# Optimization experiments

Measured on AMD Instinct MI355X. Metric: run time of the kernel, lower is better.

Reference implementation:

```python
import jax, jax.numpy as jnp
import numpy as np
from jax import lax

EPS = 1e-8
TAU = 1.0  # step=0 < tau_warmup_steps -> tau = tau_init


def setup_inputs() -> dict:
    key = jax.random.key(0)
    k1, k2 = jax.random.split(key)
    B, D, H, W = 4, 256, 32, 32
    C, K, d = 8, 1024, 32  # n_codebooks, vocab_size, codebook_dim (D = C*d)
    z = jax.random.normal(k1, (B, D, H, W), dtype=jnp.float32)
    cb = jax.random.normal(k2, (C, K, d), dtype=jnp.float32)
    cb = cb / (jnp.linalg.norm(cb, axis=-1, keepdims=True) + 1e-12) * np.sqrt(d).astype(np.float32)
    return {"z": z, "codebooks": cb}


def reference(z, codebooks):
    # Training-mode forward of LGQuantizer (step=0).
    B, D, H, W = z.shape
    C, K, d = codebooks.shape
    # (b d h w) -> (b h w) (c d_sub): chunk along channel dim
    zf = z.transpose(0, 2, 3, 1).reshape(-1, C, d)  # [N, C, d]
    N = zf.shape[0]

    # pairwise squared distances per codebook: [N, C, K]
    z_sq = jnp.sum(zf * zf, axis=-1)                      # [N, C]
    cb_sq = jnp.sum(codebooks * codebooks, axis=-1)       # [C, K]
    cross = jnp.einsum('ncd,ckd->nck', zf, codebooks)     # [N, C, K]
    dists = z_sq[:, :, None] - 2.0 * cross + cb_sq[None, :, :]

    inv_temp = 1.0 / (2.0 * TAU * TAU + EPS)
    logits = -dists * inv_temp
    q = jax.nn.softmax(logits, axis=-1)                   # [N, C, K]

    # soft quantization + straight-through with hard lookup
    z_q = jnp.einsum('nck,ckd->ncd', q, codebooks)        # [N, C, d]
    idx = jnp.argmin(dists, axis=-1)                      # [N, C]
    z_q_hard = codebooks[jnp.arange(C)[None, :], idx]     # [N, C, d]
    z_q_st = z_q + lax.stop_gradient(z_q_hard - z_q)

    quantized = z_q_st.reshape(B, H, W, D).transpose(0, 3, 1, 2)  # [B, D, H, W]
    indices = idx.reshape(B, H, W, C).transpose(0, 3, 1, 2)       # [B, C, H, W]

    # commitment: mse(z_part, q.detach() @ cb.detach()), averaged over codebooks
    commitment = jnp.mean((zf - lax.stop_gradient(z_q)) ** 2)

    log_q = jnp.log(q + EPS)
    neg_ent = jnp.sum(q * log_q, axis=-1)                 # [N, C]
    expected_dist = jnp.mean(jnp.sum(q * dists, axis=-1), axis=0)  # [C]
    kl_uniform = jnp.mean(neg_ent, axis=0) + np.log(K).astype(np.float32)  # [C]
    free_energy = jnp.mean(expected_dist * inv_temp + kl_uniform)

    confidence_loss = jnp.mean(-neg_ent)

    q_bar = jnp.mean(q, axis=0)                           # [C, K]
    balance_loss = jnp.mean(jnp.sum(q_bar * jnp.log(q_bar * K + EPS), axis=-1))

    return (quantized, indices, q, commitment, free_energy,
            confidence_loss, balance_loss, jnp.float32(TAU))
```

## Files before the change

kernel.cpp:

```cpp
#include <hip/hip_runtime.h>

#define WS_A0 0
#define WS_A1 1
#define WS_A2 2
#define WS_QBAR 16
#define WS_CBSQ (WS_QBAR + 8192)
#define WS_IDX  (WS_CBSQ + 8192)

#define OUT_IDX  1048576
#define OUT_Q    1081344
#define OUT_SCAL 34635776

__global__ __launch_bounds__(256) void k_cbsq(const float* __restrict__ cb,
                                              float* __restrict__ ws_f) {
  int i = blockIdx.x * 256 + threadIdx.x;
  const float* r = cb + (size_t)i * 32;
  float s = 0.f;
#pragma unroll
  for (int d = 0; d < 32; ++d) s = fmaf(r[d], r[d], s);
  ws_f[WS_CBSQ + i] = s;
}

__device__ __forceinline__ float wsum64(float v) {
#pragma unroll
  for (int m = 32; m >= 1; m >>= 1) v += __shfl_xor(v, m, 64);
  return v;
}

__device__ __forceinline__ float uread(float v) {
  return __int_as_float(__builtin_amdgcn_readfirstlane(__float_as_int(v)));
}

#define ZLD 33
__global__ __launch_bounds__(1024, 4)
void k_main(
    const float* __restrict__ z, const float* __restrict__ cb,
    float* __restrict__ out, float* __restrict__ ws_f, int* __restrict__ ws_i) {
  __shared__ __attribute__((aligned(16))) float smem[39040];
  float* cb_lds   = smem;
  float* qsum     = smem + 32768;
  float* cbsq_lds = smem + 33792;
  float* z_lds    = smem + 34816;

  const int c    = blockIdx.x >> 5;
  const int nblk = blockIdx.x & 31;
  const int tid  = threadIdx.x;
  const int lane = tid & 63;
  const int wave = tid >> 6;

  const int bb   = (nblk * 128) >> 10;
  const int hwb  = (nblk * 128) & 1023;

  const float4* cb4 = (const float4*)(cb + (size_t)c * 32768);
  float4* lds4 = (float4*)cb_lds;
#pragma unroll
  for (int i = 0; i < 8; ++i) {
    int idx = i * 1024 + tid;
    int k = idx >> 3, q = idx & 7;
    lds4[(k << 3) + (q ^ (k & 7))] = cb4[idx];
  }
  qsum[tid] = 0.f;
  cbsq_lds[tid] = ws_f[WS_CBSQ + c * 1024 + tid];
  {
    const float* zbase = z + (((size_t)bb * 256 + c * 32) << 10) + hwb;
#pragma unroll
    for (int i = 0; i < 4; ++i) {
      int idx = i * 1024 + tid;
      int d = idx >> 7, j = idx & 127;
      z_lds[j * ZLD + d] = zbase[(size_t)d * 1024 + j];
    }
  }
  __syncthreads();

  float* out_q   = out + OUT_Q;
  float* out_idx = out + OUT_IDX;

  float accA0 = 0.f, accA1 = 0.f, accA2 = 0.f;
  const int kl7 = lane & 7;

#pragma unroll 1
  for (int pp = 0; pp < 4; ++pp) {
    const int nl0 = wave * 8 + pp * 2;
    const int nl1 = nl0 + 1;
    const int n0 = nblk * 128 + nl0;
    const int n1 = n0 + 1;

    float zv0[32], zv1[32];
#pragma unroll
    for (int d = 0; d < 32; ++d) {
      zv0[d] = uread(z_lds[nl0 * ZLD + d]);
      zv1[d] = uread(z_lds[nl1 * ZLD + d]);
    }
    float zs0 = 0.f, zs1 = 0.f;
#pragma unroll
    for (int d = 0; d < 32; ++d) {
      zs0 = fmaf(zv0[d], zv0[d], zs0);
      zs1 = fmaf(zv1[d], zv1[d], zs1);
    }

    float S0 = 0.f, S1 = 0.f, es0 = 0.f, es1 = 0.f;
    float zqA0[16], zqA1[16];
#pragma unroll
    for (int i = 0; i < 16; ++i) { zqA0[i] = 0.f; zqA1[i] = 0.f; }

#pragma unroll 1
    for (int jj = 0; jj < 16; ++jj) {
      const int k = jj * 64 + lane;
      const int kbase = k << 3;
      float a0 = 0.f, a1 = 0.f, g0 = 0.f, g1 = 0.f;
#pragma unroll
      for (int q = 0; q < 8; ++q) {
        float4 r4 = lds4[kbase + (q ^ kl7)];
        a0 = fmaf(r4.x, zv0[q * 4 + 0], a0);
        a1 = fmaf(r4.y, zv0[q * 4 + 1], a1);
        a0 = fmaf(r4.z, zv0[q * 4 + 2], a0);
        a1 = fmaf(r4.w, zv0[q * 4 + 3], a1);
        g0 = fmaf(r4.x, zv1[q * 4 + 0], g0);
        g1 = fmaf(r4.y, zv1[q * 4 + 1], g1);
        g0 = fmaf(r4.z, zv1[q * 4 + 2], g0);
        g1 = fmaf(r4.w, zv1[q * 4 + 3], g1);
      }
      float cq = cbsq_lds[k];
      float s0 = (a0 + a1) - 0.5f * cq;
      float s1 = (g0 + g1) - 0.5f * cq;
      float ev0 = __expf(s0), ev1 = __expf(s1);
      S0 += ev0;  S1 += ev1;
      es0 = fmaf(ev0, s0, es0);
      es1 = fmaf(ev1, s1, es1);
#pragma unroll
      for (int q = 0; q < 4; ++q) {
        float4 r4 = lds4[kbase + (q ^ kl7)];
        zqA0[q * 4 + 0] = fmaf(ev0, r4.x, zqA0[q * 4 + 0]);
        zqA0[q * 4 + 1] = fmaf(ev0, r4.y, zqA0[q * 4 + 1]);
        zqA0[q * 4 + 2] = fmaf(ev0, r4.z, zqA0[q * 4 + 2]);
        zqA0[q * 4 + 3] = fmaf(ev0, r4.w, zqA0[q * 4 + 3]);
        zqA1[q * 4 + 0] = fmaf(ev1, r4.x, zqA1[q * 4 + 0]);
        zqA1[q * 4 + 1] = fmaf(ev1, r4.y, zqA1[q * 4 + 1]);
        zqA1[q * 4 + 2] = fmaf(ev1, r4.z, zqA1[q * 4 + 2]);
        zqA1[q * 4 + 3] = fmaf(ev1, r4.w, zqA1[q * 4 + 3]);
      }
    }

    float St0 = wsum64(S0), St1 = wsum64(S1);
    float rS0 = 1.f / St0, rS1 = 1.f / St1;
    float est0 = wsum64(es0), est1 = wsum64(es1);

    accA1 += (zs0 - 2.f * est0 * rS0) + (zs1 - 2.f * est1 * rS1);
    accA2 += (est0 * rS0 - __logf(St0)) + (est1 * rS1 - __logf(St1));

    {
#pragma unroll
      for (int t = 0; t < 4; ++t) {
        const int half = 8 >> t;
        const int up = (lane >> (5 - t)) & 1;
#pragma unroll
        for (int i = 0; i < half; ++i) {
          float sa0 = up ? zqA0[i] : zqA0[i + half];
          float ka0 = up ? zqA0[i + half] : zqA0[i];
          zqA0[i] = ka0 + __shfl_xor(sa0, 32 >> t, 64);
          float sa1 = up ? zqA1[i] : zqA1[i + half];
          float ka1 = up ? zqA1[i + half] : zqA1[i];
          zqA1[i] = ka1 + __shfl_xor(sa1, 32 >> t, 64);
        }
      }
      zqA0[0] += __shfl_xor(zqA0[0], 2, 64);
      zqA0[0] += __shfl_xor(zqA0[0], 1, 64);
      zqA1[0] += __shfl_xor(zqA1[0], 2, 64);
      zqA1[0] += __shfl_xor(zqA1[0], 1, 64);
      const int ddA = (lane >> 2) & 15;
      float dA0 = z_lds[nl0 * ZLD + ddA] - zqA0[0] * rS0;
      float dA1 = z_lds[nl1 * ZLD + ddA] - zqA1[0] * rS1;
      accA0 += 0.25f * wsum64(dA0 * dA0 + dA1 * dA1);
    }

    float sm0 = -INFINITY, sm1 = -INFINITY;
    int km0 = 0, km1 = 0;
    float zqB0[16], zqB1[16];
#pragma unroll
    for (int i = 0; i < 16; ++i) { zqB0[i] = 0.f; zqB1[i] = 0.f; }
    float* qp0 = out_q + ((size_t)n0 * 8 + c) * 1024;
    float* qp1 = out_q + ((size_t)n1 * 8 + c) * 1024;

#pragma unroll 1
    for (int jj = 0; jj < 16; ++jj) {
      const int k = jj * 64 + lane;
      const int kbase = k << 3;
      float a0 = 0.f, a1 = 0.f, g0 = 0.f, g1 = 0.f;
#pragma unroll
      for (int q = 0; q < 8; ++q) {
        float4 r4 = lds4[kbase + (q ^ kl7)];
        a0 = fmaf(r4.x, zv0[q * 4 + 0], a0);
        a1 = fmaf(r4.y, zv0[q * 4 + 1], a1);
        a0 = fmaf(r4.z, zv0[q * 4 + 2], a0);
        a1 = fmaf(r4.w, zv0[q * 4 + 3], a1);
        g0 = fmaf(r4.x, zv1[q * 4 + 0], g0);
        g1 = fmaf(r4.y, zv1[q * 4 + 1], g1);
        g0 = fmaf(r4.z, zv1[q * 4 + 2], g0);
        g1 = fmaf(r4.w, zv1[q * 4 + 3], g1);
      }
      float cq = cbsq_lds[k];
      float s0 = (a0 + a1) - 0.5f * cq;
      float s1 = (g0 + g1) - 0.5f * cq;
      if (s0 > sm0) { sm0 = s0; km0 = k; }
      if (s1 > sm1) { sm1 = s1; km1 = k; }
      float qv0 = __expf(s0) * rS0;
      float qv1 = __expf(s1) * rS1;
      __builtin_nontemporal_store(qv0, qp0 + jj * 64 + lane);
      __builtin_nontemporal_store(qv1, qp1 + jj * 64 + lane);
      atomicAdd(&qsum[jj * 64 + lane], qv0 + qv1);
#pragma unroll
      for (int q = 4; q < 8; ++q) {
        float4 r4 = lds4[kbase + (q ^ kl7)];
        const int i0 = (q - 4) * 4;
        zqB0[i0 + 0] = fmaf(qv0, r4.x, zqB0[i0 + 0]);
        zqB0[i0 + 1] = fmaf(qv0, r4.y, zqB0[i0 + 1]);
        zqB0[i0 + 2] = fmaf(qv0, r4.z, zqB0[i0 + 2]);
        zqB0[i0 + 3] = fmaf(qv0, r4.w, zqB0[i0 + 3]);
        zqB1[i0 + 0] = fmaf(qv1, r4.x, zqB1[i0 + 0]);
        zqB1[i0 + 1] = fmaf(qv1, r4.y, zqB1[i0 + 1]);
        zqB1[i0 + 2] = fmaf(qv1, r4.z, zqB1[i0 + 2]);
        zqB1[i0 + 3] = fmaf(qv1, r4.w, zqB1[i0 + 3]);
      }
    }

#pragma unroll
    for (int m = 32; m >= 1; m >>= 1) {
      float so = __shfl_xor(sm0, m, 64); int ko = __shfl_xor(km0, m, 64);
      if (so > sm0 || (so == sm0 && ko < km0)) { sm0 = so; km0 = ko; }
      float sp = __shfl_xor(sm1, m, 64); int kp = __shfl_xor(km1, m, 64);
      if (sp > sm1 || (sp == sm1 && kp < km1)) { sm1 = sp; km1 = kp; }
    }
    if (lane == 0) {
      out_idx[(size_t)bb * 8192 + c * 1024 + hwb + nl0] = (float)km0;
      ws_i[WS_IDX + n0 * 8 + c] = km0;
      out_idx[(size_t)bb * 8192 + c * 1024 + hwb + nl1] = (float)km1;
      ws_i[WS_IDX + n1 * 8 + c] = km1;
    }

#pragma unroll
    for (int t = 0; t < 4; ++t) {
      const int half = 8 >> t;
      const int up = (lane >> (5 - t)) & 1;
#pragma unroll
      for (int i = 0; i < half; ++i) {
        float sa0 = up ? zqB0[i] : zqB0[i + half];
        float ka0 = up ? zqB0[i + half] : zqB0[i];
        zqB0[i] = ka0 + __shfl_xor(sa0, 32 >> t, 64);
        float sa1 = up ? zqB1[i] : zqB1[i + half];
        float ka1 = up ? zqB1[i + half] : zqB1[i];
        zqB1[i] = ka1 + __shfl_xor(sa1, 32 >> t, 64);
      }
    }
    zqB0[0] += __shfl_xor(zqB0[0], 2, 64);
    zqB0[0] += __shfl_xor(zqB0[0], 1, 64);
    zqB1[0] += __shfl_xor(zqB1[0], 2, 64);
    zqB1[0] += __shfl_xor(zqB1[0], 1, 64);
    const int ddB = (lane >> 2) & 15;
    float dB0 = z_lds[nl0 * ZLD + 16 + ddB] - zqB0[0];
    float dB1 = z_lds[nl1 * ZLD + 16 + ddB] - zqB1[0];
    accA0 += 0.25f * wsum64(dB0 * dB0 + dB1 * dB1);
  }

  if (lane == 0) {
    atomicAdd(&ws_f[WS_A0], accA0);
    atomicAdd(&ws_f[WS_A1], accA1);
    atomicAdd(&ws_f[WS_A2], accA2);
  }

  __syncthreads();
  atomicAdd(&ws_f[WS_QBAR + c * 1024 + tid], qsum[tid]);
}

__global__ __launch_bounds__(256) void k_hard(const float* __restrict__ cb,
                                              const int* __restrict__ ws_i,
                                              float* __restrict__ out0) {
  int o = blockIdx.x * 256 + threadIdx.x;
  int b  = o >> 18;
  int r  = o & 262143;
  int ch = r >> 10;
  int hw = r & 1023;
  int c = ch >> 5, dd = ch & 31;
  int n = (b << 10) + hw;
  int k = ws_i[WS_IDX + n * 8 + c];
  out0[o] = cb[((size_t)(c << 10) + k) * 32 + dd];
}

__global__ __launch_bounds__(256) void k_final(const float* __restrict__ ws_f,
                                               float* __restrict__ out_s) {
  __shared__ float red[256];
  int tid = threadIdx.x;
  float bal = 0.f;
  for (int i = tid; i < 8192; i += 256) {
    float qb = ws_f[WS_QBAR + i] * (1.0f / 4096.0f);
    bal += qb * __logf(qb * 1024.0f + 1e-8f);
  }
  red[tid] = bal;
  __syncthreads();
  for (int s = 128; s > 0; s >>= 1) {
    if (tid < s) red[tid] += red[tid + s];
    __syncthreads();
  }
  if (tid == 0) {
    float A0 = ws_f[WS_A0], A1 = ws_f[WS_A1], A2 = ws_f[WS_A2];
    out_s[0] = A0 * (1.0f / 1048576.0f);
    out_s[1] = (0.5f * A1 + A2) * (1.0f / 32768.0f) + 6.93147180559945f;
    out_s[2] = -A2 * (1.0f / 32768.0f);
    out_s[3] = red[0] * 0.125f;
    out_s[4] = 1.0f;
  }
}

extern "C" void kernel_launch(void* const* d_in, const int* in_sizes, int n_in,
                              void* d_out, int out_size, void* d_ws, size_t ws_size,
                              hipStream_t stream) {
  (void)in_sizes; (void)n_in; (void)out_size; (void)ws_size;
  const float* z  = (const float*)d_in[0];
  const float* cb = (const float*)d_in[1];
  float* out  = (float*)d_out;
  float* ws_f = (float*)d_ws;
  int*   ws_i = (int*)d_ws;

  hipMemsetAsync(d_ws, 0, (WS_QBAR + 8192) * sizeof(float), stream);
  k_cbsq <<<32,   256, 0, stream>>>(cb, ws_f);
  k_main <<<256, 1024, 0, stream>>>(z, cb, out, ws_f, ws_i);
  k_hard <<<4096, 256, 0, stream>>>(cb, ws_i, out);
  k_final<<<1,    256, 0, stream>>>(ws_f, out + OUT_SCAL);
}
```

Measured before the change: 481.7 us.

## Fuse cbsq into main kernel, fold final reduction into hard lookup, reuse codebook loads

```diff
diff --git a/kernel.cpp b/kernel.cpp
--- a/kernel.cpp
+++ b/kernel.cpp
@@ -10,16 +10,6 @@
 #define OUT_IDX  1048576
 #define OUT_Q    1081344
 #define OUT_SCAL 34635776
-
-__global__ __launch_bounds__(256) void k_cbsq(const float* __restrict__ cb,
-                                              float* __restrict__ ws_f) {
-  int i = blockIdx.x * 256 + threadIdx.x;
-  const float* r = cb + (size_t)i * 32;
-  float s = 0.f;
-#pragma unroll
-  for (int d = 0; d < 32; ++d) s = fmaf(r[d], r[d], s);
-  ws_f[WS_CBSQ + i] = s;
-}
 
 __device__ __forceinline__ float wsum64(float v) {
 #pragma unroll
@@ -60,7 +50,6 @@
     lds4[(k << 3) + (q ^ (k & 7))] = cb4[idx];
   }
   qsum[tid] = 0.f;
-  cbsq_lds[tid] = ws_f[WS_CBSQ + c * 1024 + tid];
   {
     const float* zbase = z + (((size_t)bb * 256 + c * 32) << 10) + hwb;
 #pragma unroll
@@ -69,6 +58,18 @@
       int d = idx >> 7, j = idx & 127;
       z_lds[j * ZLD + d] = zbase[(size_t)d * 1024 + j];
     }
+  }
+  __syncthreads();
+  {
+    float s = 0.f;
+    const int t7 = tid & 7;
+#pragma unroll
+    for (int q = 0; q < 8; ++q) {
+      float4 r4 = lds4[(tid << 3) + (q ^ t7)];
+      s = fmaf(r4.x, r4.x, s); s = fmaf(r4.y, r4.y, s);
+      s = fmaf(r4.z, r4.z, s); s = fmaf(r4.w, r4.w, s);
+    }
+    cbsq_lds[tid] = s;
   }
   __syncthreads();
 
@@ -109,7 +110,8 @@
       const int kbase = k << 3;
       float a0 = 0.f, a1 = 0.f, g0 = 0.f, g1 = 0.f;
 #pragma unroll
-      for (int q = 0; q < 8; ++q) {
+      for (int qq = 0; qq < 6; ++qq) {
+        const int q = (qq + 4) & 7;
         float4 r4 = lds4[kbase + (q ^ kl7)];
         a0 = fmaf(r4.x, zv0[q * 4 + 0], a0);
         a1 = fmaf(r4.y, zv0[q * 4 + 1], a1);
@@ -120,6 +122,17 @@
         g0 = fmaf(r4.z, zv1[q * 4 + 2], g0);
         g1 = fmaf(r4.w, zv1[q * 4 + 3], g1);
       }
+      float4 kq2 = lds4[kbase + (2 ^ kl7)];
+      a0 = fmaf(kq2.x, zv0[8], a0);  a1 = fmaf(kq2.y, zv0[9], a1);
+      a0 = fmaf(kq2.z, zv0[10], a0); a1 = fmaf(kq2.w, zv0[11], a1);
+      g0 = fmaf(kq2.x, zv1[8], g0);  g1 = fmaf(kq2.y, zv1[9], g1);
+      g0 = fmaf(kq2.z, zv1[10], g0); g1 = fmaf(kq2.w, zv1[11], g1);
+      float4 kq3 = lds4[kbase + (3 ^ kl7)];
+      a0 = fmaf(kq3.x, zv0[12], a0); a1 = fmaf(kq3.y, zv0[13], a1);
+      a0 = fmaf(kq3.z, zv0[14], a0); a1 = fmaf(kq3.w, zv0[15], a1);
+      g0 = fmaf(kq3.x, zv1[12], g0); g1 = fmaf(kq3.y, zv1[13], g1);
+      g0 = fmaf(kq3.z, zv1[14], g0); g1 = fmaf(kq3.w, zv1[15], g1);
+
       float cq = cbsq_lds[k];
       float s0 = (a0 + a1) - 0.5f * cq;
       float s1 = (g0 + g1) - 0.5f * cq;
@@ -128,7 +141,7 @@
       es0 = fmaf(ev0, s0, es0);
       es1 = fmaf(ev1, s1, es1);
 #pragma unroll
-      for (int q = 0; q < 4; ++q) {
+      for (int q = 0; q < 2; ++q) {
         float4 r4 = lds4[kbase + (q ^ kl7)];
         zqA0[q * 4 + 0] = fmaf(ev0, r4.x, zqA0[q * 4 + 0]);
         zqA0[q * 4 + 1] = fmaf(ev0, r4.y, zqA0[q * 4 + 1]);
@@ -139,6 +152,14 @@
         zqA1[q * 4 + 2] = fmaf(ev1, r4.z, zqA1[q * 4 + 2]);
         zqA1[q * 4 + 3] = fmaf(ev1, r4.w, zqA1[q * 4 + 3]);
       }
+      zqA0[8]  = fmaf(ev0, kq2.x, zqA0[8]);  zqA0[9]  = fmaf(ev0, kq2.y, zqA0[9]);
+      zqA0[10] = fmaf(ev0, kq2.z, zqA0[10]); zqA0[11] = fmaf(ev0, kq2.w, zqA0[11]);
+      zqA1[8]  = fmaf(ev1, kq2.x, zqA1[8]);  zqA1[9]  = fmaf(ev1, kq2.y, zqA1[9]);
+      zqA1[10] = fmaf(ev1, kq2.z, zqA1[10]); zqA1[11] = fmaf(ev1, kq2.w, zqA1[11]);
+      zqA0[12] = fmaf(ev0, kq3.x, zqA0[12]); zqA0[13] = fmaf(ev0, kq3.y, zqA0[13]);
+      zqA0[14] = fmaf(ev0, kq3.z, zqA0[14]); zqA0[15] = fmaf(ev0, kq3.w, zqA0[15]);
+      zqA1[12] = fmaf(ev1, kq3.x, zqA1[12]); zqA1[13] = fmaf(ev1, kq3.y, zqA1[13]);
+      zqA1[14] = fmaf(ev1, kq3.z, zqA1[14]); zqA1[15] = fmaf(ev1, kq3.w, zqA1[15]);
     }
 
     float St0 = wsum64(S0), St1 = wsum64(S1);
@@ -187,7 +208,7 @@
       const int kbase = k << 3;
       float a0 = 0.f, a1 = 0.f, g0 = 0.f, g1 = 0.f;
 #pragma unroll
-      for (int q = 0; q < 8; ++q) {
+      for (int q = 0; q < 6; ++q) {
         float4 r4 = lds4[kbase + (q ^ kl7)];
         a0 = fmaf(r4.x, zv0[q * 4 + 0], a0);
         a1 = fmaf(r4.y, zv0[q * 4 + 1], a1);
@@ -198,6 +219,17 @@
         g0 = fmaf(r4.z, zv1[q * 4 + 2], g0);
         g1 = fmaf(r4.w, zv1[q * 4 + 3], g1);
       }
+      float4 kq6 = lds4[kbase + (6 ^ kl7)];
+      a0 = fmaf(kq6.x, zv0[24], a0); a1 = fmaf(kq6.y, zv0[25], a1);
+      a0 = fmaf(kq6.z, zv0[26], a0); a1 = fmaf(kq6.w, zv0[27], a1);
+      g0 = fmaf(kq6.x, zv1[24], g0); g1 = fmaf(kq6.y, zv1[25], g1);
+      g0 = fmaf(kq6.z, zv1[26], g0); g1 = fmaf(kq6.w, zv1[27], g1);
+      float4 kq7 = lds4[kbase + (7 ^ kl7)];
+      a0 = fmaf(kq7.x, zv0[28], a0); a1 = fmaf(kq7.y, zv0[29], a1);
+      a0 = fmaf(kq7.z, zv0[30], a0); a1 = fmaf(kq7.w, zv0[31], a1);
+      g0 = fmaf(kq7.x, zv1[28], g0); g1 = fmaf(kq7.y, zv1[29], g1);
+      g0 = fmaf(kq7.z, zv1[30], g0); g1 = fmaf(kq7.w, zv1[31], g1);
+
       float cq = cbsq_lds[k];
       float s0 = (a0 + a1) - 0.5f * cq;
       float s1 = (g0 + g1) - 0.5f * cq;
@@ -209,7 +241,7 @@
       __builtin_nontemporal_store(qv1, qp1 + jj * 64 + lane);
       atomicAdd(&qsum[jj * 64 + lane], qv0 + qv1);
 #pragma unroll
-      for (int q = 4; q < 8; ++q) {
+      for (int q = 4; q < 6; ++q) {
         float4 r4 = lds4[kbase + (q ^ kl7)];
         const int i0 = (q - 4) * 4;
         zqB0[i0 + 0] = fmaf(qv0, r4.x, zqB0[i0 + 0]);
@@ -221,6 +253,14 @@
         zqB1[i0 + 2] = fmaf(qv1, r4.z, zqB1[i0 + 2]);
         zqB1[i0 + 3] = fmaf(qv1, r4.w, zqB1[i0 + 3]);
       }
+      zqB0[8]  = fmaf(qv0, kq6.x, zqB0[8]);  zqB0[9]  = fmaf(qv0, kq6.y, zqB0[9]);
+      zqB0[10] = fmaf(qv0, kq6.z, zqB0[10]); zqB0[11] = fmaf(qv0, kq6.w, zqB0[11]);
+      zqB1[8]  = fmaf(qv1, kq6.x, zqB1[8]);  zqB1[9]  = fmaf(qv1, kq6.y, zqB1[9]);
+      zqB1[10] = fmaf(qv1, kq6.z, zqB1[10]); zqB1[11] = fmaf(qv1, kq6.w, zqB1[11]);
+      zqB0[12] = fmaf(qv0, kq7.x, zqB0[12]); zqB0[13] = fmaf(qv0, kq7.y, zqB0[13]);
+      zqB0[14] = fmaf(qv0, kq7.z, zqB0[14]); zqB0[15] = fmaf(qv0, kq7.w, zqB0[15]);
+      zqB1[12] = fmaf(qv1, kq7.x, zqB1[12]); zqB1[13] = fmaf(qv1, kq7.y, zqB1[13]);
+      zqB1[14] = fmaf(qv1, kq7.z, zqB1[14]); zqB1[15] = fmaf(qv1, kq7.w, zqB1[15]);
     }
 
 #pragma unroll
@@ -273,7 +313,9 @@
 
 __global__ __launch_bounds__(256) void k_hard(const float* __restrict__ cb,
                                               const int* __restrict__ ws_i,
-                                              float* __restrict__ out0) {
+                                              float* __restrict__ out0,
+                                              const float* __restrict__ ws_f,
+                                              float* __restrict__ out_s) {
   int o = blockIdx.x * 256 + threadIdx.x;
   int b  = o >> 18;
   int r  = o & 262143;
@@ -283,30 +325,29 @@
   int n = (b << 10) + hw;
   int k = ws_i[WS_IDX + n * 8 + c];
   out0[o] = cb[((size_t)(c << 10) + k) * 32 + dd];
-}
-
-__global__ __launch_bounds__(256) void k_final(const float* __restrict__ ws_f,
-                                               float* __restrict__ out_s) {
-  __shared__ float red[256];
-  int tid = threadIdx.x;
-  float bal = 0.f;
-  for (int i = tid; i < 8192; i += 256) {
-    float qb = ws_f[WS_QBAR + i] * (1.0f / 4096.0f);
-    bal += qb * __logf(qb * 1024.0f + 1e-8f);
-  }
-  red[tid] = bal;
-  __syncthreads();
-  for (int s = 128; s > 0; s >>= 1) {
-    if (tid < s) red[tid] += red[tid + s];
+
+  if (blockIdx.x == 0) {
+    __shared__ float red[256];
+    int tid = threadIdx.x;
+    float bal = 0.f;
+    for (int i = tid; i < 8192; i += 256) {
+      float qb = ws_f[WS_QBAR + i] * (1.0f / 4096.0f);
+      bal += qb * __logf(qb * 1024.0f + 1e-8f);
+    }
+    red[tid] = bal;
     __syncthreads();
-  }
-  if (tid == 0) {
-    float A0 = ws_f[WS_A0], A1 = ws_f[WS_A1], A2 = ws_f[WS_A2];
-    out_s[0] = A0 * (1.0f / 1048576.0f);
-    out_s[1] = (0.5f * A1 + A2) * (1.0f / 32768.0f) + 6.93147180559945f;
-    out_s[2] = -A2 * (1.0f / 32768.0f);
-    out_s[3] = red[0] * 0.125f;
-    out_s[4] = 1.0f;
+    for (int s = 128; s > 0; s >>= 1) {
+      if (tid < s) red[tid] += red[tid + s];
+      __syncthreads();
+    }
+    if (tid == 0) {
+      float A0 = ws_f[WS_A0], A1 = ws_f[WS_A1], A2 = ws_f[WS_A2];
+      out_s[0] = A0 * (1.0f / 1048576.0f);
+      out_s[1] = (0.5f * A1 + A2) * (1.0f / 32768.0f) + 6.93147180559945f;
+      out_s[2] = -A2 * (1.0f / 32768.0f);
+      out_s[3] = red[0] * 0.125f;
+      out_s[4] = 1.0f;
+    }
   }
 }
 
@@ -321,8 +362,6 @@
   int*   ws_i = (int*)d_ws;
 
   hipMemsetAsync(d_ws, 0, (WS_QBAR + 8192) * sizeof(float), stream);
-  k_cbsq <<<32,   256, 0, stream>>>(cb, ws_f);
   k_main <<<256, 1024, 0, stream>>>(z, cb, out, ws_f, ws_i);
-  k_hard <<<4096, 256, 0, stream>>>(cb, ws_i, out);
-  k_final<<<1,    256, 0, stream>>>(ws_f, out + OUT_SCAL);
-}
+  k_hard <<<4096, 256, 0, stream>>>(cb, ws_i, out, ws_f, out + OUT_SCAL);
+}
```

Result: faster. 448.4 us (-6.9%).
